# Performance work log

Hardware: AMD Instinct MI355X
Metric: run time of the kernel (lower is better)

## Reference

```python
import jax, jax.numpy as jnp
import numpy as np

VOCAB = 50000
N_TOPICS = 200
EMB = 512
BATCH = 2048
TOPK = 20


def setup_inputs() -> dict:
    key = jax.random.key(0)
    k1, k2, k3, k4 = jax.random.split(key, 4)
    alpha = jax.random.normal(k1, (BATCH, N_TOPICS), dtype=jnp.float32)
    doc_bow = jax.random.uniform(k2, (BATCH, VOCAB), dtype=jnp.float32)
    # learned parameters (orthogonal init in the original; scaled normal is fine for a numeric reference)
    topic_embeddings_mat = jax.random.normal(k3, (N_TOPICS, EMB), dtype=jnp.float32) * 0.05
    word_embeddings_mat = jax.random.normal(k4, (EMB, VOCAB), dtype=jnp.float32) * 0.05
    return {
        "alpha": alpha,
        "doc_bow": doc_bow,
        "topic_embeddings_mat": topic_embeddings_mat,
        "word_embeddings_mat": word_embeddings_mat,
    }


def _topk_filter_norm(beta, k):
    # keep top-k entries per topic row, scatter back to [T, V], renormalize to sum 1
    vals, idx = jax.lax.top_k(beta, k)           # [T, k]
    T = beta.shape[0]
    rows = jnp.arange(T)[:, None]
    sparse = jnp.zeros_like(beta).at[rows, idx].set(vals)
    return sparse / vals.sum(-1, keepdims=True)  # [T, V]


def _stdr(beta, k, n_topics):
    # geomloss Sinkhorn(p=2) on single-point clouds == ||x - y||^2 / 2 per pair.
    # Original double loop: sum_{i,j} C(b_i, b_j) / n_topics^2 -> Gram-matrix trick.
    b = _topk_filter_norm(beta, k)               # [T, V]
    sq = jnp.sum(b * b, axis=-1)                 # [T]
    gram = b @ b.T                               # [T, T]
    d2 = jnp.maximum(sq[:, None] + sq[None, :] - 2.0 * gram, 0.0)
    cost = 0.5 * d2
    return cost.sum() / (n_topics * n_topics)


def reference(alpha, doc_bow, topic_embeddings_mat, word_embeddings_mat):
    theta = jax.nn.softmax(alpha, axis=-1)                         # [B, T]
    wt = topic_embeddings_mat @ word_embeddings_mat                # [T, V]
    beta = jax.nn.softmax(wt, axis=1)                              # softmax over vocab
    logits = jnp.log(theta @ beta)                                 # [B, V]
    Re = -jnp.sum(logits * doc_bow, axis=-1)                       # [B]
    STDR = _stdr(beta, TOPK, N_TOPICS)
    return Re, STDR, theta
```

## Files before the change

### kernel.cpp

```cpp
#include <hip/hip_runtime.h>
#include <hip/hip_bf16.h>

#define VOCAB 50000
#define NT    200
#define NTP   256
#define EMB   512
#define BATCH 2048
#define KP    224
#define TK    20

typedef __bf16 bf16x8 __attribute__((ext_vector_type(8)));
typedef float  f32x4  __attribute__((ext_vector_type(4)));

#define OFF_EXPWT   0ull
#define OFF_BETA    40000000ull
#define OFF_THETAB  62400000ull
#define OFF_TOPICA  63317504ull
#define OFF_ROWSUM  63579648ull
#define OFF_STDR    63580448ull
#define OFF_TKV     63580464ull
#define OFF_TKI     63596464ull
#define OFF_TKSQ    63612464ull

__global__ __launch_bounds__(64) void k_theta(const float* __restrict__ alpha,
                                              float* __restrict__ theta_out,
                                              __bf16* __restrict__ theta_b) {
    int b = blockIdx.x;
    int ln = threadIdx.x;
    const float* row = alpha + (size_t)b * NT;
    float a0 = row[ln], a1 = row[ln + 64], a2 = row[ln + 128];
    float a3 = (ln < 8) ? row[ln + 192] : -1e30f;
    float m = fmaxf(fmaxf(a0, a1), fmaxf(a2, a3));
    #pragma unroll
    for (int off = 32; off; off >>= 1) m = fmaxf(m, __shfl_xor(m, off));
    float e0 = __expf(a0 - m), e1 = __expf(a1 - m), e2 = __expf(a2 - m);
    float e3 = (ln < 8) ? __expf(a3 - m) : 0.f;
    float s = e0 + e1 + e2 + e3;
    #pragma unroll
    for (int off = 32; off; off >>= 1) s += __shfl_xor(s, off);
    float inv = 1.f / s;
    float* o = theta_out + (size_t)b * NT;
    __bf16* ob = theta_b + (size_t)b * KP;
    o[ln]       = e0 * inv;  ob[ln]       = (__bf16)(e0 * inv);
    o[ln + 64]  = e1 * inv;  ob[ln + 64]  = (__bf16)(e1 * inv);
    o[ln + 128] = e2 * inv;  ob[ln + 128] = (__bf16)(e2 * inv);
    if (ln < 8)       { o[ln + 192] = e3 * inv; ob[ln + 192] = (__bf16)(e3 * inv); }
    else if (ln < 32) { ob[ln + 192] = (__bf16)0.f; }
}

__global__ __launch_bounds__(256) void k_topic_cvt(const float* __restrict__ te,
                                                   __bf16* __restrict__ out) {
    int i = blockIdx.x * 256 + threadIdx.x;
    int t = i >> 9, k = i & 511;
    out[i] = (t < NT) ? (__bf16)te[(size_t)t * EMB + k] : (__bf16)0.f;
}

__global__ __launch_bounds__(256) void k_gemm1(const float* __restrict__ wemb,
                                               const __bf16* __restrict__ Abf,
                                               float* __restrict__ expwt,
                                               float* __restrict__ rowsum) {
    __shared__ __align__(16) __bf16 lA[NTP * 40];
    __shared__ __align__(16) __bf16 lB[64 * 40];
    int tid = threadIdx.x;
    int v0 = blockIdx.x * 64;
    int w = tid >> 6, ln = tid & 63, quad = ln >> 4, c16 = ln & 15;

    f32x4 acc[4][4];
    #pragma unroll
    for (int mi = 0; mi < 4; ++mi)
        #pragma unroll
        for (int ni = 0; ni < 4; ++ni) acc[mi][ni] = (f32x4){0.f, 0.f, 0.f, 0.f};

    for (int ks = 0; ks < EMB / 32; ++ks) {
        int k0 = ks * 32;
        __syncthreads();
        {
            const uint4* src = (const uint4*)(Abf + (size_t)tid * EMB + k0);
            uint4* dst = (uint4*)(&lA[tid * 40]);
            dst[0] = src[0]; dst[1] = src[1]; dst[2] = src[2]; dst[3] = src[3];
        }
        {
            int c = tid & 63, kg = tid >> 6;
            int v = v0 + c;
            bool ok = (v < VOCAB);
            #pragma unroll
            for (int it = 0; it < 8; ++it) {
                int k = kg * 8 + it;
                float val = ok ? wemb[(size_t)(k0 + k) * VOCAB + v] : 0.f;
                lB[c * 40 + k] = (__bf16)val;
            }
        }
        __syncthreads();
        bf16x8 aF[4], bF[4];
        #pragma unroll
        for (int mi = 0; mi < 4; ++mi)
            aF[mi] = *(const bf16x8*)(&lA[(w * 64 + mi * 16 + c16) * 40 + quad * 8]);
        #pragma unroll
        for (int ni = 0; ni < 4; ++ni)
            bF[ni] = *(const bf16x8*)(&lB[(ni * 16 + c16) * 40 + quad * 8]);
        #pragma unroll
        for (int mi = 0; mi < 4; ++mi)
            #pragma unroll
            for (int ni = 0; ni < 4; ++ni)
                acc[mi][ni] = __builtin_amdgcn_mfma_f32_16x16x32_bf16(aF[mi], bF[ni], acc[mi][ni], 0, 0, 0);
    }

    #pragma unroll
    for (int mi = 0; mi < 4; ++mi) {
        #pragma unroll
        for (int r = 0; r < 4; ++r) {
            int tt = w * 64 + mi * 16 + quad * 4 + r;
            float rs = 0.f;
            if (tt < NT) {
                #pragma unroll
                for (int ni = 0; ni < 4; ++ni) {
                    int v = v0 + ni * 16 + c16;
                    if (v < VOCAB) {
                        float e = __expf(acc[mi][ni][r]);
                        expwt[(size_t)tt * VOCAB + v] = e;
                        rs += e;
                    }
                }
            }
            #pragma unroll
            for (int off = 1; off < 16; off <<= 1) rs += __shfl_xor(rs, off, 16);
            if (tt < NT && c16 == 0) atomicAdd(&rowsum[tt], rs);
        }
    }
}

__global__ __launch_bounds__(256) void k_norm(const float* __restrict__ expwt,
                                              const float* __restrict__ rowsum,
                                              __bf16* __restrict__ beta) {
    int t = blockIdx.y;
    int v = blockIdx.x * 256 + threadIdx.x;
    if (v >= VOCAB) return;
    float out = 0.f;
    if (t < NT) out = expwt[(size_t)t * VOCAB + v] * (1.f / rowsum[t]);
    beta[(size_t)t * VOCAB + v] = (__bf16)out;
}

__global__ __launch_bounds__(256) void k_gemm2(const __bf16* __restrict__ thetab,
                                               const __bf16* __restrict__ beta,
                                               const float* __restrict__ bow,
                                               float* __restrict__ Re) {
    __shared__ __align__(16) __bf16 lA[128 * 40];
    __shared__ __align__(16) __bf16 lB[128 * 40];
    int tid = threadIdx.x;
    int m0 = blockIdx.x * 128;
    int v0 = blockIdx.y * 128;
    int w = tid >> 6, ln = tid & 63, quad = ln >> 4, c16 = ln & 15;

    f32x4 acc[2][8];
    #pragma unroll
    for (int mi = 0; mi < 2; ++mi)
        #pragma unroll
        for (int ni = 0; ni < 8; ++ni) acc[mi][ni] = (f32x4){0.f, 0.f, 0.f, 0.f};

    for (int ks = 0; ks < KP / 32; ++ks) {
        int k0 = ks * 32;
        __syncthreads();
        {
            #pragma unroll
            for (int i = 0; i < 2; ++i) {
                int u = tid * 2 + i;
                int row = u >> 2, seg = u & 3;
                *(uint4*)(&lA[row * 40 + seg * 8]) =
                    *(const uint4*)(thetab + (size_t)(m0 + row) * KP + k0 + seg * 8);
            }
        }
        {
            int c = tid & 127, kg = tid >> 7;
            int v = v0 + c;
            bool ok = (v < VOCAB);
            #pragma unroll
            for (int it = 0; it < 16; ++it) {
                int k = kg * 16 + it;
                __bf16 val = ok ? beta[(size_t)(k0 + k) * VOCAB + v] : (__bf16)0.f;
                lB[c * 40 + k] = val;
            }
        }
        __syncthreads();
        bf16x8 aF[2], bF[8];
        #pragma unroll
        for (int mi = 0; mi < 2; ++mi)
            aF[mi] = *(const bf16x8*)(&lA[(w * 32 + mi * 16 + c16) * 40 + quad * 8]);
        #pragma unroll
        for (int ni = 0; ni < 8; ++ni)
            bF[ni] = *(const bf16x8*)(&lB[(ni * 16 + c16) * 40 + quad * 8]);
        #pragma unroll
        for (int mi = 0; mi < 2; ++mi)
            #pragma unroll
            for (int ni = 0; ni < 8; ++ni)
                acc[mi][ni] = __builtin_amdgcn_mfma_f32_16x16x32_bf16(aF[mi], bF[ni], acc[mi][ni], 0, 0, 0);
    }

    #pragma unroll
    for (int mi = 0; mi < 2; ++mi) {
        #pragma unroll
        for (int r = 0; r < 4; ++r) {
            int b = m0 + w * 32 + mi * 16 + quad * 4 + r;
            float s = 0.f;
            #pragma unroll
            for (int ni = 0; ni < 8; ++ni) {
                int v = v0 + ni * 16 + c16;
                if (v < VOCAB)
                    s += __logf(acc[mi][ni][r]) * bow[(size_t)b * VOCAB + v];
            }
            #pragma unroll
            for (int off = 1; off < 16; off <<= 1) s += __shfl_xor(s, off, 16);
            if (c16 == 0) atomicAdd(&Re[b], -s);
        }
    }
}

__global__ __launch_bounds__(256) void k_topk(const float* __restrict__ expwt,
                                              float* __restrict__ tkv,
                                              int* __restrict__ tki,
                                              float* __restrict__ tksq) {
    __shared__ float lv[256 * TK];
    __shared__ int   li[256 * TK];
    __shared__ int   head[256];
    __shared__ float redv[256];
    __shared__ int   redi[256];
    __shared__ float selv[TK];
    __shared__ int   seli[TK];
    int t = blockIdx.x, tid = threadIdx.x;
    const float* row = expwt + (size_t)t * VOCAB;

    float tv[TK]; int ti[TK];
    #pragma unroll
    for (int i = 0; i < TK; ++i) { tv[i] = -1e30f; ti[i] = 0; }

    for (int v = tid; v < VOCAB; v += 256) {
        float val = row[v];
        if (val > tv[TK - 1]) {
            #pragma unroll
            for (int i = TK - 1; i >= 1; --i) {
                bool sh  = val > tv[i - 1];
                bool put = val > tv[i];
                float nv = sh ? tv[i - 1] : (put ? val : tv[i]);
                int  nix = sh ? ti[i - 1] : (put ? v   : ti[i]);
                tv[i] = nv; ti[i] = nix;
            }
            if (val > tv[0]) { tv[0] = val; ti[0] = v; }
        }
    }
    #pragma unroll
    for (int i = 0; i < TK; ++i) { lv[tid * TK + i] = tv[i]; li[tid * TK + i] = ti[i]; }
    head[tid] = 0;
    __syncthreads();

    for (int sel = 0; sel < TK; ++sel) {
        int h = head[tid];
        redv[tid] = (h < TK) ? lv[tid * TK + h] : -1e30f;
        redi[tid] = tid;
        __syncthreads();
        for (int s2 = 128; s2 > 0; s2 >>= 1) {
            if (tid < s2) {
                if (redv[tid + s2] > redv[tid]) {
                    redv[tid] = redv[tid + s2]; redi[tid] = redi[tid + s2];
                }
            }
            __syncthreads();
        }
        if (tid == 0) {
            int wt = redi[0];
            int hh = head[wt];
            selv[sel] = lv[wt * TK + hh];
            seli[sel] = li[wt * TK + hh];
            head[wt] = hh + 1;
        }
        __syncthreads();
    }

    if (tid == 0) {
        float sum = 0.f;
        #pragma unroll
        for (int i = 0; i < TK; ++i) sum += selv[i];
        float inv = 1.f / sum, sq = 0.f;
        #pragma unroll
        for (int i = 0; i < TK; ++i) {
            float nv = selv[i] * inv;
            tkv[t * TK + i] = nv;
            tki[t * TK + i] = seli[i];
            sq += nv * nv;
        }
        tksq[t] = sq;
    }
}

__global__ __launch_bounds__(256) void k_pairs(const float* __restrict__ tkv,
                                               const int* __restrict__ tki,
                                               const float* __restrict__ tksq,
                                               float* __restrict__ stdr) {
    int p = blockIdx.x * 256 + threadIdx.x;
    float contrib = 0.f;
    if (p < NT * NT) {
        int i = p / NT, j = p % NT;
        float vi[TK], vj[TK]; int ii[TK], ij[TK];
        #pragma unroll
        for (int a = 0; a < TK; ++a) { vi[a] = tkv[i * TK + a]; ii[a] = tki[i * TK + a]; }
        #pragma unroll
        for (int a = 0; a < TK; ++a) { vj[a] = tkv[j * TK + a]; ij[a] = tki[j * TK + a]; }
        float g = 0.f;
        for (int a = 0; a < TK; ++a) {
            #pragma unroll
            for (int b = 0; b < TK; ++b)
                if (ii[a] == ij[b]) g += vi[a] * vj[b];
        }
        float d2 = fmaxf(tksq[i] + tksq[j] - 2.f * g, 0.f);
        contrib = 0.5f * d2;
    }
    __shared__ float red[256];
    red[threadIdx.x] = contrib;
    __syncthreads();
    for (int s = 128; s; s >>= 1) {
        if (threadIdx.x < s) red[threadIdx.x] += red[threadIdx.x + s];
        __syncthreads();
    }
    if (threadIdx.x == 0) atomicAdd(stdr, red[0]);
}

__global__ void k_final(const float* __restrict__ stdr, float* __restrict__ out) {
    out[0] = stdr[0] * (1.f / (float)(NT * NT));
}

extern "C" void kernel_launch(void* const* d_in, const int* in_sizes, int n_in,
                              void* d_out, int out_size, void* d_ws, size_t ws_size,
                              hipStream_t stream) {
    const float* alpha = (const float*)d_in[0];
    const float* bow   = (const float*)d_in[1];
    const float* temb  = (const float*)d_in[2];
    const float* wemb  = (const float*)d_in[3];
    float* out = (float*)d_out;
    char* ws = (char*)d_ws;

    float*  expwt  = (float*)(ws + OFF_EXPWT);
    __bf16* beta   = (__bf16*)(ws + OFF_BETA);
    __bf16* thetab = (__bf16*)(ws + OFF_THETAB);
    __bf16* topA   = (__bf16*)(ws + OFF_TOPICA);
    float*  rowsum = (float*)(ws + OFF_ROWSUM);
    float*  stdr   = (float*)(ws + OFF_STDR);
    float*  tkv    = (float*)(ws + OFF_TKV);
    int*    tki    = (int*)(ws + OFF_TKI);
    float*  tksq   = (float*)(ws + OFF_TKSQ);

    float* Re        = out;
    float* stdr_out  = out + BATCH;
    float* theta_out = out + BATCH + 1;

    hipMemsetAsync(Re, 0, BATCH * sizeof(float), stream);
    hipMemsetAsync(ws + OFF_ROWSUM, 0, 804, stream);

    k_theta<<<BATCH, 64, 0, stream>>>(alpha, theta_out, thetab);
    k_topic_cvt<<<512, 256, 0, stream>>>(temb, topA);
    k_gemm1<<<(VOCAB + 63) / 64, 256, 0, stream>>>(wemb, topA, expwt, rowsum);
    k_norm<<<dim3((VOCAB + 255) / 256, KP), 256, 0, stream>>>(expwt, rowsum, beta);
    k_gemm2<<<dim3(BATCH / 128, (VOCAB + 127) / 128), 256, 0, stream>>>(thetab, beta, bow, Re);
    k_topk<<<NT, 256, 0, stream>>>(expwt, tkv, tki, tksq);
    k_pairs<<<(NT * NT + 255) / 256, 256, 0, stream>>>(tkv, tki, tksq, stdr);
    k_final<<<1, 1, 0, stream>>>(stdr, stdr_out);
}
```

Baseline: 1.404 ms.

## Store beta transposed in bf16 and split top-k into two stages

The exp(wt) buffer is stored as bf16 instead of fp32, which halves that write/read traffic. A new normalization kernel transposes beta into a [V, KP] layout so GEMM2 can load B tiles with 16-byte vector loads instead of scalar strided loads. Top-k now runs in two passes: per-chunk candidate selection over the transposed beta, then a wave-level merge. The risk is bf16 rounding of the exp values feeding top-k selection and the row sums, plus uncoalesced per-topic column reads in the first top-k pass.

Measured after the change: 2.238 ms. 1.59x slower.

```diff
diff --git a/kernel.cpp b/kernel.cpp
--- a/kernel.cpp
+++ b/kernel.cpp
@@ -8,19 +8,24 @@
 #define BATCH 2048
 #define KP    224
 #define TK    20
+#define NB1   50
+#define VCHUNK 1000
+#define NCAND (NB1 * TK)
 
 typedef __bf16 bf16x8 __attribute__((ext_vector_type(8)));
 typedef float  f32x4  __attribute__((ext_vector_type(4)));
 
 #define OFF_EXPWT   0ull
-#define OFF_BETA    40000000ull
-#define OFF_THETAB  62400000ull
-#define OFF_TOPICA  63317504ull
-#define OFF_ROWSUM  63579648ull
-#define OFF_STDR    63580448ull
-#define OFF_TKV     63580464ull
-#define OFF_TKI     63596464ull
-#define OFF_TKSQ    63612464ull
+#define OFF_BETA    20000000ull
+#define OFF_THETAB  42400000ull
+#define OFF_TOPICA  43317504ull
+#define OFF_ROWSUM  43579648ull
+#define OFF_STDR    43580448ull
+#define OFF_TKV     43580464ull
+#define OFF_TKI     43596464ull
+#define OFF_TKSQ    43612464ull
+#define OFF_CANDV   43613264ull
+#define OFF_CANDI   44413264ull
 
 __global__ __launch_bounds__(64) void k_theta(const float* __restrict__ alpha,
                                               float* __restrict__ theta_out,
@@ -57,7 +62,7 @@
 
 __global__ __launch_bounds__(256) void k_gemm1(const float* __restrict__ wemb,
                                                const __bf16* __restrict__ Abf,
-                                               float* __restrict__ expwt,
+                                               __bf16* __restrict__ expwt,
                                                float* __restrict__ rowsum) {
     __shared__ __align__(16) __bf16 lA[NTP * 40];
     __shared__ __align__(16) __bf16 lB[64 * 40];
@@ -83,12 +88,14 @@
             int c = tid & 63, kg = tid >> 6;
             int v = v0 + c;
             bool ok = (v < VOCAB);
+            __align__(16) __bf16 tmp[8];
             #pragma unroll
             for (int it = 0; it < 8; ++it) {
                 int k = kg * 8 + it;
                 float val = ok ? wemb[(size_t)(k0 + k) * VOCAB + v] : 0.f;
-                lB[c * 40 + k] = (__bf16)val;
+                tmp[it] = (__bf16)val;
             }
+            *(uint4*)(&lB[c * 40 + kg * 8]) = *(const uint4*)tmp;
         }
         __syncthreads();
         bf16x8 aF[4], bF[4];
@@ -117,7 +124,7 @@
                     int v = v0 + ni * 16 + c16;
                     if (v < VOCAB) {
                         float e = __expf(acc[mi][ni][r]);
-                        expwt[(size_t)tt * VOCAB + v] = e;
+                        expwt[(size_t)tt * VOCAB + v] = (__bf16)e;
                         rs += e;
                     }
                 }
@@ -129,19 +136,40 @@
     }
 }
 
-__global__ __launch_bounds__(256) void k_norm(const float* __restrict__ expwt,
-                                              const float* __restrict__ rowsum,
-                                              __bf16* __restrict__ beta) {
-    int t = blockIdx.y;
-    int v = blockIdx.x * 256 + threadIdx.x;
-    if (v >= VOCAB) return;
-    float out = 0.f;
-    if (t < NT) out = expwt[(size_t)t * VOCAB + v] * (1.f / rowsum[t]);
-    beta[(size_t)t * VOCAB + v] = (__bf16)out;
+__global__ __launch_bounds__(256) void k_norm_t(const __bf16* __restrict__ expwt,
+                                                const float* __restrict__ rowsum,
+                                                __bf16* __restrict__ beta_t) {
+    __shared__ float tile[KP * 65];
+    int tid = threadIdx.x;
+    int v0 = blockIdx.x * 64;
+    int vsub = tid & 63, tq = tid >> 6;
+    #pragma unroll 4
+    for (int t0 = 0; t0 < KP; t0 += 4) {
+        int t = t0 + tq;
+        float val = 0.f;
+        int v = v0 + vsub;
+        if (t < NT && v < VOCAB)
+            val = (float)expwt[(size_t)t * VOCAB + v] * (1.f / rowsum[t]);
+        tile[t * 65 + vsub] = val;
+    }
+    __syncthreads();
+    #pragma unroll
+    for (int i = 0; i < 7; ++i) {
+        int u = tid + i * 256;
+        int r = u / 28;
+        int c = (u % 28) * 8;
+        int v = v0 + r;
+        if (v < VOCAB) {
+            __align__(16) __bf16 tmp[8];
+            #pragma unroll
+            for (int j = 0; j < 8; ++j) tmp[j] = (__bf16)tile[(c + j) * 65 + r];
+            *(uint4*)(beta_t + (size_t)v * KP + c) = *(const uint4*)tmp;
+        }
+    }
 }
 
 __global__ __launch_bounds__(256) void k_gemm2(const __bf16* __restrict__ thetab,
-                                               const __bf16* __restrict__ beta,
+                                               const __bf16* __restrict__ beta_t,
                                                const float* __restrict__ bow,
                                                float* __restrict__ Re) {
     __shared__ __align__(16) __bf16 lA[128 * 40];
@@ -160,25 +188,22 @@
     for (int ks = 0; ks < KP / 32; ++ks) {
         int k0 = ks * 32;
         __syncthreads();
-        {
-            #pragma unroll
-            for (int i = 0; i < 2; ++i) {
-                int u = tid * 2 + i;
-                int row = u >> 2, seg = u & 3;
-                *(uint4*)(&lA[row * 40 + seg * 8]) =
-                    *(const uint4*)(thetab + (size_t)(m0 + row) * KP + k0 + seg * 8);
-            }
-        }
-        {
-            int c = tid & 127, kg = tid >> 7;
-            int v = v0 + c;
-            bool ok = (v < VOCAB);
-            #pragma unroll
-            for (int it = 0; it < 16; ++it) {
-                int k = kg * 16 + it;
-                __bf16 val = ok ? beta[(size_t)(k0 + k) * VOCAB + v] : (__bf16)0.f;
-                lB[c * 40 + k] = val;
-            }
+        #pragma unroll
+        for (int i = 0; i < 2; ++i) {
+            int u = tid + i * 256;
+            int row = u >> 2, seg = u & 3;
+            *(uint4*)(&lA[row * 40 + seg * 8]) =
+                *(const uint4*)(thetab + (size_t)(m0 + row) * KP + k0 + seg * 8);
+        }
+        #pragma unroll
+        for (int i = 0; i < 2; ++i) {
+            int u = tid + i * 256;
+            int row = u >> 2, seg = u & 3;
+            int v = v0 + row;
+            uint4 val;
+            if (v < VOCAB) val = *(const uint4*)(beta_t + (size_t)v * KP + k0 + seg * 8);
+            else           val = make_uint4(0u, 0u, 0u, 0u);
+            *(uint4*)(&lB[row * 40 + seg * 8]) = val;
         }
         __syncthreads();
         bf16x8 aF[2], bF[8];
@@ -214,26 +239,21 @@
     }
 }
 
-__global__ __launch_bounds__(256) void k_topk(const float* __restrict__ expwt,
-                                              float* __restrict__ tkv,
-                                              int* __restrict__ tki,
-                                              float* __restrict__ tksq) {
-    __shared__ float lv[256 * TK];
-    __shared__ int   li[256 * TK];
-    __shared__ int   head[256];
-    __shared__ float redv[256];
-    __shared__ int   redi[256];
-    __shared__ float selv[TK];
-    __shared__ int   seli[TK];
-    int t = blockIdx.x, tid = threadIdx.x;
-    const float* row = expwt + (size_t)t * VOCAB;
+__global__ __launch_bounds__(256) void k_topk1(const __bf16* __restrict__ beta_t,
+                                               float* __restrict__ candv,
+                                               int* __restrict__ candi) {
+    int t = threadIdx.x;
+    int blk = blockIdx.x;
+    int v0 = blk * VCHUNK;
+    if (t >= NT) return;
 
     float tv[TK]; int ti[TK];
     #pragma unroll
-    for (int i = 0; i < TK; ++i) { tv[i] = -1e30f; ti[i] = 0; }
-
-    for (int v = tid; v < VOCAB; v += 256) {
-        float val = row[v];
+    for (int i = 0; i < TK; ++i) { tv[i] = -1e30f; ti[i] = 0x7fffffff; }
+
+    for (int dv = 0; dv < VCHUNK; ++dv) {
+        int v = v0 + dv;
+        float val = (float)beta_t[(size_t)v * KP + t];
         if (val > tv[TK - 1]) {
             #pragma unroll
             for (int i = TK - 1; i >= 1; --i) {
@@ -246,48 +266,72 @@
             if (val > tv[0]) { tv[0] = val; ti[0] = v; }
         }
     }
-    #pragma unroll
-    for (int i = 0; i < TK; ++i) { lv[tid * TK + i] = tv[i]; li[tid * TK + i] = ti[i]; }
-    head[tid] = 0;
+    float* ov = candv + ((size_t)t * NB1 + blk) * TK;
+    int*   oi = candi + ((size_t)t * NB1 + blk) * TK;
+    #pragma unroll
+    for (int i = 0; i < TK; ++i) { ov[i] = tv[i]; oi[i] = ti[i]; }
+}
+
+__global__ __launch_bounds__(64) void k_topk2(const float* __restrict__ candv,
+                                              const int* __restrict__ candi,
+                                              float* __restrict__ tkv,
+                                              int* __restrict__ tki,
+                                              float* __restrict__ tksq) {
+    __shared__ float wv[TK];
+    __shared__ int   wi[TK];
+    int t = blockIdx.x, ln = threadIdx.x;
+    const float* cv = candv + (size_t)t * NCAND;
+    const int*   ci = candi + (size_t)t * NCAND;
+
+    float tv[TK]; int ti[TK];
+    #pragma unroll
+    for (int i = 0; i < TK; ++i) { tv[i] = -1e30f; ti[i] = 0x7fffffff; }
+
+    for (int i = ln; i < NCAND; i += 64) {
+        float val = cv[i]; int idx = ci[i];
+        if (val > tv[TK - 1]) {
+            #pragma unroll
+            for (int k = TK - 1; k >= 1; --k) {
+                bool sh  = val > tv[k - 1];
+                bool put = val > tv[k];
+                float nv = sh ? tv[k - 1] : (put ? val : tv[k]);
+                int  nix = sh ? ti[k - 1] : (put ? idx : ti[k]);
+                tv[k] = nv; ti[k] = nix;
+            }
+            if (val > tv[0]) { tv[0] = val; ti[0] = idx; }
+        }
+    }
+
+    float sum = 0.f;
+    for (int sel = 0; sel < TK; ++sel) {
+        float bv = tv[0]; int bi = ti[0]; int bl = ln;
+        #pragma unroll
+        for (int off = 32; off; off >>= 1) {
+            float ov = __shfl_xor(bv, off);
+            int   oi = __shfl_xor(bi, off);
+            int   ol = __shfl_xor(bl, off);
+            bool take = (ov > bv) || (ov == bv && oi < bi);
+            if (take) { bv = ov; bi = oi; bl = ol; }
+        }
+        if (ln == bl) {
+            #pragma unroll
+            for (int i = 0; i < TK - 1; ++i) { tv[i] = tv[i + 1]; ti[i] = ti[i + 1]; }
+            tv[TK - 1] = -1e30f; ti[TK - 1] = 0x7fffffff;
+        }
+        if (ln == 0) { wv[sel] = bv; wi[sel] = bi; }
+        sum += bv;
+    }
     __syncthreads();
-
-    for (int sel = 0; sel < TK; ++sel) {
-        int h = head[tid];
-        redv[tid] = (h < TK) ? lv[tid * TK + h] : -1e30f;
-        redi[tid] = tid;
-        __syncthreads();
-        for (int s2 = 128; s2 > 0; s2 >>= 1) {
-            if (tid < s2) {
-                if (redv[tid + s2] > redv[tid]) {
-                    redv[tid] = redv[tid + s2]; redi[tid] = redi[tid + s2];
-                }
-            }
-            __syncthreads();
-        }
-        if (tid == 0) {
-            int wt = redi[0];
-            int hh = head[wt];
-            selv[sel] = lv[wt * TK + hh];
-            seli[sel] = li[wt * TK + hh];
-            head[wt] = hh + 1;
-        }
-        __syncthreads();
-    }
-
-    if (tid == 0) {
-        float sum = 0.f;
-        #pragma unroll
-        for (int i = 0; i < TK; ++i) sum += selv[i];
-        float inv = 1.f / sum, sq = 0.f;
-        #pragma unroll
-        for (int i = 0; i < TK; ++i) {
-            float nv = selv[i] * inv;
-            tkv[t * TK + i] = nv;
-            tki[t * TK + i] = seli[i];
-            sq += nv * nv;
-        }
-        tksq[t] = sq;
-    }
+    float inv = 1.f / sum;
+    float nv = (ln < TK) ? wv[ln] * inv : 0.f;
+    if (ln < TK) {
+        tkv[t * TK + ln] = nv;
+        tki[t * TK + ln] = wi[ln];
+    }
+    float sq = nv * nv;
+    #pragma unroll
+    for (int off = 32; off; off >>= 1) sq += __shfl_xor(sq, off);
+    if (ln == 0) tksq[t] = sq;
 }
 
 __global__ __launch_bounds__(256) void k_pairs(const float* __restrict__ tkv,
@@ -336,8 +380,8 @@
     float* out = (float*)d_out;
     char* ws = (char*)d_ws;
 
-    float*  expwt  = (float*)(ws + OFF_EXPWT);
-    __bf16* beta   = (__bf16*)(ws + OFF_BETA);
+    __bf16* expwt  = (__bf16*)(ws + OFF_EXPWT);
+    __bf16* beta_t = (__bf16*)(ws + OFF_BETA);
     __bf16* thetab = (__bf16*)(ws + OFF_THETAB);
     __bf16* topA   = (__bf16*)(ws + OFF_TOPICA);
     float*  rowsum = (float*)(ws + OFF_ROWSUM);
@@ -345,20 +389,23 @@
     float*  tkv    = (float*)(ws + OFF_TKV);
     int*    tki    = (int*)(ws + OFF_TKI);
     float*  tksq   = (float*)(ws + OFF_TKSQ);
+    float*  candv  = (float*)(ws + OFF_CANDV);
+    int*    candi  = (int*)(ws + OFF_CANDI);
 
     float* Re        = out;
     float* stdr_out  = out + BATCH;
     float* theta_out = out + BATCH + 1;
 
     hipMemsetAsync(Re, 0, BATCH * sizeof(float), stream);
-    hipMemsetAsync(ws + OFF_ROWSUM, 0, 804, stream);
+    hipMemsetAsync(ws + OFF_ROWSUM, 0, 820, stream);
 
     k_theta<<<BATCH, 64, 0, stream>>>(alpha, theta_out, thetab);
     k_topic_cvt<<<512, 256, 0, stream>>>(temb, topA);
     k_gemm1<<<(VOCAB + 63) / 64, 256, 0, stream>>>(wemb, topA, expwt, rowsum);
-    k_norm<<<dim3((VOCAB + 255) / 256, KP), 256, 0, stream>>>(expwt, rowsum, beta);
-    k_gemm2<<<dim3(BATCH / 128, (VOCAB + 127) / 128), 256, 0, stream>>>(thetab, beta, bow, Re);
-    k_topk<<<NT, 256, 0, stream>>>(expwt, tkv, tki, tksq);
+    k_norm_t<<<(VOCAB + 63) / 64, 256, 0, stream>>>(expwt, rowsum, beta_t);
+    k_gemm2<<<dim3(BATCH / 128, (VOCAB + 127) / 128), 256, 0, stream>>>(thetab, beta_t, bow, Re);
+    k_topk1<<<NB1, 256, 0, stream>>>(beta_t, candv, candi);
+    k_topk2<<<NT, 64, 0, stream>>>(candv, candi, tkv, tki, tksq);
     k_pairs<<<(NT * NT + 255) / 256, 256, 0, stream>>>(tkv, tki, tksq, stdr);
     k_final<<<1, 1, 0, stream>>>(stdr, stdr_out);
 }
```
